# Kernel tuning notes

Hardware: AMD Instinct MI355X
Metric: run time of the kernel (lower is better)

Reference implementation:

```python
import jax, jax.numpy as jnp
import numpy as np

B, N, C = 2, 2048, 768
H, HD = 12, 64
HID = 3072
LN_EPS = 1e-5
POL_EPS = 1e-6


def _layer_norm(x, g, b):
    m = jnp.mean(x, axis=-1, keepdims=True)
    v = jnp.mean(jnp.square(x - m), axis=-1, keepdims=True)
    return (x - m) * jax.lax.rsqrt(v + LN_EPS) * g + b


def _softmax_with_policy(attn, policy):
    # attn: [B,H,N,N], policy: [B,N,1]
    n = attn.shape[-1]
    ap = policy.reshape(policy.shape[0], 1, 1, n)  # [B,1,1,N]
    eye = jnp.eye(n, dtype=ap.dtype)[None, None]   # [1,1,N,N]
    ap = ap + (1.0 - ap) * eye                     # always attend to self
    attn = attn - jnp.max(attn, axis=-1, keepdims=True)
    attn = jnp.exp(attn.astype(jnp.float32)) * ap.astype(jnp.float32)
    attn = (attn + POL_EPS / n) / (jnp.sum(attn, axis=-1, keepdims=True) + POL_EPS)
    return attn


def setup_inputs() -> dict:
    key = jax.random.key(0)
    ks = jax.random.split(key, 12)
    s = lambda fan_in: 1.0 / np.sqrt(fan_in)
    x = jax.random.normal(ks[0], (B, N, C), dtype=jnp.float32)
    policy = (jax.random.uniform(ks[1], (B, N, 1)) > 0.5).astype(jnp.float32)
    return {
        "x": x,
        "policy": policy,
        "ln1_g": jnp.ones((C,), jnp.float32),
        "ln1_b": jnp.zeros((C,), jnp.float32),
        "qkv_w": jax.random.uniform(ks[2], (3 * H * HD, C), jnp.float32, -s(C), s(C)),
        "proj_w": jax.random.uniform(ks[3], (C, H * HD), jnp.float32, -s(H * HD), s(H * HD)),
        "proj_b": jnp.zeros((C,), jnp.float32),
        "ln2_g": jnp.ones((C,), jnp.float32),
        "ln2_b": jnp.zeros((C,), jnp.float32),
        "fc1_w": jax.random.uniform(ks[4], (HID, C), jnp.float32, -s(C), s(C)),
        "fc1_b": jnp.zeros((HID,), jnp.float32),
        "fc2_w": jax.random.uniform(ks[5], (C, HID), jnp.float32, -s(HID), s(HID)),
        "fc2_b": jnp.zeros((C,), jnp.float32),
    }


def reference(x, policy, ln1_g, ln1_b, qkv_w, proj_w, proj_b, ln2_g, ln2_b, fc1_w, fc1_b, fc2_w, fc2_b):
    b, n, c = x.shape
    scale = HD ** -0.5
    # --- attention branch (pre-LN) ---
    h = _layer_norm(x, ln1_g, ln1_b)
    qkv = (h @ qkv_w.T).reshape(b, n, 3, H, HD).transpose(2, 0, 3, 1, 4)  # [3,B,H,N,hd]
    q, k, v = qkv[0], qkv[1], qkv[2]
    attn = jnp.einsum("bhqd,bhkd->bhqk", q * scale, k)
    attn = _softmax_with_policy(attn, policy).astype(x.dtype)
    o = jnp.einsum("bhqk,bhkd->bhqd", attn, v).transpose(0, 2, 1, 3).reshape(b, n, H * HD)
    x = x + (o @ proj_w.T + proj_b)  # skip_lam = 1.0, dropout/drop_path = identity
    # --- MLP branch (pre-LN) ---
    h = _layer_norm(x, ln2_g, ln2_b)
    h = jax.nn.gelu(h @ fc1_w.T + fc1_b, approximate=False)  # torch nn.GELU = exact erf
    x = x + (h @ fc2_w.T + fc2_b)
    return x
```

## Files before the change

### kernel.cpp

```cpp
#include <hip/hip_runtime.h>

typedef unsigned short u16;
typedef unsigned int u32;
typedef float f32x4 __attribute__((ext_vector_type(4)));
typedef float f32x16 __attribute__((ext_vector_type(16)));
typedef __bf16 bf16x8 __attribute__((ext_vector_type(8)));
typedef u16 u16x4v __attribute__((ext_vector_type(4)));
typedef u32 u32x2 __attribute__((ext_vector_type(2)));
typedef u32 u32x4 __attribute__((ext_vector_type(4)));

#define NHEAD 12
#define NN 2048
#define CC 768

#define GLOBAL_AS __attribute__((address_space(1)))
#define LDS_AS __attribute__((address_space(3)))

__device__ __forceinline__ u16 tobf(float f) {
  __bf16 h = (__bf16)f;
  return __builtin_bit_cast(u16, h);
}
__device__ __forceinline__ float bf2f(u16 h) {
  u32 u = ((u32)h) << 16;
  return __builtin_bit_cast(float, u);
}
__device__ __forceinline__ u32 cvtpk(float lo, float hi) {
  u32 r;
  asm("v_cvt_pk_bf16_f32 %0, %1, %2" : "=v"(r) : "v"(lo), "v"(hi));
  return r;
}
__device__ __forceinline__ void plswap(u32& a, u32& b) {
  asm volatile("v_permlane32_swap_b32 %0, %1" : "+v"(a), "+v"(b));
}
__device__ __forceinline__ void plswapf(float& a, float& b) {
  asm volatile("v_permlane32_swap_b32 %0, %1" : "+v"(a), "+v"(b));
}
__device__ __forceinline__ float gelu_erf(float v) {
  float y = fabsf(v) * 0.70710678118654752f;
  float t = __builtin_amdgcn_rcpf(fmaf(0.3275911f, y, 1.f));
  float p = fmaf(1.061405429f, t, -1.453152027f);
  p = fmaf(p, t, 1.421413741f);
  p = fmaf(p, t, -0.284496736f);
  p = fmaf(p, t, 0.254829592f);
  p = p * t;
  float e = __builtin_amdgcn_exp2f(-y * y * 1.44269504f);
  float er = fmaf(-p, e, 1.f);
  er = (v < 0.f) ? -er : er;
  return 0.5f * v * (1.f + er);
}

#define N4_QKV 442368
#define N4_PROJ 147456
#define N4_FC 589824
__global__ __launch_bounds__(256) void cvt4_kernel(
    const float* __restrict__ a, const float* __restrict__ b,
    const float* __restrict__ c, const float* __restrict__ d,
    u16* __restrict__ oa, u16* __restrict__ ob, u16* __restrict__ oc,
    u16* __restrict__ od) {
  int i = blockIdx.x * 256 + threadIdx.x;
  const float* src;
  u16* dst;
  if (i < N4_QKV) {
    src = a; dst = oa;
  } else if (i < N4_QKV + N4_PROJ) {
    i -= N4_QKV; src = b; dst = ob;
  } else if (i < N4_QKV + N4_PROJ + N4_FC) {
    i -= N4_QKV + N4_PROJ; src = c; dst = oc;
  } else {
    i -= N4_QKV + N4_PROJ + N4_FC; src = d; dst = od;
    if (i >= N4_FC) return;
  }
  float4 v = ((const float4*)src)[i];
  u16x4v o = {tobf(v.x), tobf(v.y), tobf(v.z), tobf(v.w)};
  ((u16x4v*)dst)[i] = o;
}

__global__ __launch_bounds__(256) void ln_kernel(const float* __restrict__ x,
                                                 const float* __restrict__ gw,
                                                 const float* __restrict__ bw,
                                                 u16* __restrict__ out) {
  int row = blockIdx.x * 4 + (threadIdx.x >> 6);
  int lane = threadIdx.x & 63;
  const float* xr = x + (size_t)row * CC + lane * 12;
  float v[12];
  *(float4*)&v[0] = *(const float4*)(xr + 0);
  *(float4*)&v[4] = *(const float4*)(xr + 4);
  *(float4*)&v[8] = *(const float4*)(xr + 8);
  float s = 0.f, sq = 0.f;
#pragma unroll
  for (int j = 0; j < 12; ++j) { s += v[j]; sq += v[j] * v[j]; }
#pragma unroll
  for (int o = 1; o < 64; o <<= 1) { s += __shfl_xor(s, o); sq += __shfl_xor(sq, o); }
  float mean = s * (1.f / CC);
  float var = sq * (1.f / CC) - mean * mean;
  float rs = rsqrtf(var + 1e-5f);
  u16 ob[12];
#pragma unroll
  for (int j = 0; j < 12; ++j) {
    int c = lane * 12 + j;
    ob[j] = tobf((v[j] - mean) * rs * gw[c] + bw[c]);
  }
  u32* orow = (u32*)(out + (size_t)row * CC + lane * 12);
#pragma unroll
  for (int j = 0; j < 6; ++j) orow[j] = (u32)ob[2 * j] | ((u32)ob[2 * j + 1] << 16);
}

template <int BM, int BN, int OB, int HASB, int ACT, int RES>
__global__ __launch_bounds__(256) void gemm_kernel(
    const u16* __restrict__ A, const u16* __restrict__ Bw,
    const float* __restrict__ bias, const float* __restrict__ res,
    void* __restrict__ Cout, int M, int N, int K) {
  constexpr int MW = BM / 2;
  constexpr int MF = MW / 16;
  constexpr int NF = BN / 32;
  __shared__ __align__(16) u16 Alds[BM * 64];
  __shared__ __align__(16) u16 Blds[BN * 64];
  const int tid = threadIdx.x;
  const int lane = tid & 63, wave = tid >> 6;
  const int l15 = lane & 15, g = lane >> 4;
  const int nx = gridDim.x;
  const int flat = blockIdx.y * nx + blockIdx.x;
  const int cpx = (nx * gridDim.y) >> 3;
  const int swz = (flat & 7) * cpx + (flat >> 3);
  const int bm = (swz % nx) * BM, bn = (swz / nx) * BN;
  const int wm = (wave >> 1) * MW, wn = (wave & 1) * (BN / 2);
  f32x4 acc[MF][NF] = {};

  for (int kt = 0; kt < K; kt += 64) {
#pragma unroll
    for (int i = 0; i < BM / 32; ++i) {
      int ob_ = i * 4096 + wave * 1024;
      int lb = ob_ + lane * 16;
      int row = lb >> 7;
      int cb = (lb & 127) ^ ((row & 7) << 4);
      const u16* sa = A + (size_t)(bm + row) * K + kt + (cb >> 1);
      __builtin_amdgcn_global_load_lds((const GLOBAL_AS void*)sa,
                                       (LDS_AS void*)(Alds + (ob_ >> 1)), 16, 0, 0);
    }
#pragma unroll
    for (int i = 0; i < BN / 32; ++i) {
      int ob_ = i * 4096 + wave * 1024;
      int lb = ob_ + lane * 16;
      int row = lb >> 7;
      int cb = (lb & 127) ^ ((row & 7) << 4);
      const u16* sb = Bw + (size_t)(bn + row) * K + kt + (cb >> 1);
      __builtin_amdgcn_global_load_lds((const GLOBAL_AS void*)sb,
                                       (LDS_AS void*)(Blds + (ob_ >> 1)), 16, 0, 0);
    }
    __syncthreads();
#pragma unroll
    for (int ks = 0; ks < 2; ++ks) {
      bf16x8 af[MF], bfr[NF];
#pragma unroll
      for (int mi = 0; mi < MF; ++mi) {
        int row = wm + mi * 16 + l15;
        int cb = (ks * 64 + g * 16) ^ ((row & 7) << 4);
        af[mi] = *(const bf16x8*)&Alds[row * 64 + (cb >> 1)];
      }
#pragma unroll
// ... 19 lines not shown
      float bs = HASB ? bias[col] : 0.f;
#pragma unroll
      for (int r = 0; r < 4; ++r) {
        int rowm = bm + wm + mi * 16 + g * 4 + r;
        float v = acc[mi][ni][r] + bs;
        if (ACT) v = gelu_erf(v);
        if (RES) v += res[(size_t)rowm * N + col];
        if (OB)
          ((u16*)Cout)[(size_t)rowm * N + col] = tobf(v);
        else
          ((float*)Cout)[(size_t)rowm * N + col] = v;
      }
    }
  }
}

__global__ __launch_bounds__(256) void vsum_kernel(const u16* __restrict__ qkv,
                                                   float* __restrict__ vs) {
  int bh = blockIdx.x, q4 = blockIdx.y;
  int b = bh / NHEAD, h = bh % NHEAD;
  int d = threadIdx.x & 63, part = threadIdx.x >> 6;
  float s = 0.f;
  for (int n = q4 * 512 + part; n < q4 * 512 + 512; n += 4)
    s += bf2f(qkv[(size_t)(b * NN + n) * 2304 + 2 * CC + h * 64 + d]);
  __shared__ float red[256];
  red[threadIdx.x] = s;
  __syncthreads();
  if (threadIdx.x < 64) {
    float t = red[threadIdx.x] + red[threadIdx.x + 64] + red[threadIdx.x + 128] +
              red[threadIdx.x + 192];
    vs[q4 * (24 * 64) + bh * 64 + threadIdx.x] = t;
  }
}

__global__ __launch_bounds__(256) void scan_kernel(const float* __restrict__ policy,
                                                   int* __restrict__ ncbuf,
                                                   int* __restrict__ idxbuf) {
  int b = blockIdx.x, tid = threadIdx.x;
  float pv[8];
  *(float4*)&pv[0] = *(const float4*)&policy[b * NN + tid * 8];
  *(float4*)&pv[4] = *(const float4*)&policy[b * NN + tid * 8 + 4];
  int cnt = 0;
#pragma unroll
  for (int j = 0; j < 8; ++j) cnt += (pv[j] != 0.f) ? 1 : 0;
  __shared__ int sc[256];
  sc[tid] = cnt;
  __syncthreads();
  for (int off = 1; off < 256; off <<= 1) {
    int v = sc[tid];
    int add = (tid >= off) ? sc[tid - off] : 0;
    __syncthreads();
    sc[tid] = v + add;
    __syncthreads();
  }
  int base = sc[tid] - cnt;
#pragma unroll
  for (int j = 0; j < 8; ++j) {
    if (pv[j] != 0.f) idxbuf[b * NN + base++] = tid * 8 + j;
  }
  if (tid == 255) ncbuf[b] = sc[255];
}

__global__ __launch_bounds__(256) void gather_kernel(const u16* __restrict__ qkv,
                                                     const int* __restrict__ ncbuf,
                                                     const int* __restrict__ idxbuf,
                                                     u16* __restrict__ ckv) {
  int b = blockIdx.y;
  int nc = ncbuf[b];
  int ncp = (nc + 127) & ~127;
  int c = blockIdx.x * 256 + threadIdx.x;
  int j = c / 192, col = (c % 192) * 8;
  if (j >= ncp) return;
  uint4 val = {0, 0, 0, 0};
  if (j < nc) {
    int src = idxbuf[b * NN + j];
    val = *(const uint4*)&qkv[(size_t)(b * NN + src) * 2304 + CC + col];
  }
  *(uint4*)&ckv[(size_t)(b * NN + j) * 1536 + col] = val;
}

#define SCL2E 0.18033688f
#define TRRD(dst, addr, OFF) \
  asm volatile("ds_read_b64_tr_b16 %0, %1 offset:" OFF : "=v"(dst) : "v"(addr))

__global__ __launch_bounds__(128) void attn32_kernel(const u16* __restrict__ qkv,
                                                     const u16* __restrict__ ckv,
                                                     const int* __restrict__ ncbuf,
                                                     const float* __restrict__ policy,
                                                     const float* __restrict__ vsum,
                                                     u16* __restrict__ o) {
  __shared__ __align__(16) u16 Klds[2][4096];
  __shared__ __align__(16) u16 Vlds[2][4096];
  __shared__ float alf[2][32];
  __shared__ float4 alfe[2][32];
  const int bh = blockIdx.y, b = bh / NHEAD, h = bh % NHEAD;
  const int tid = threadIdx.x, lane = tid & 63, w = tid >> 6;
  const int l31 = lane & 31, hp = lane >> 5, b4 = (lane >> 4) & 1;
  const int q0 = blockIdx.x * 64 + w * 32;
  const int nc = ncbuf[b];
  const int ncp = (nc + 127) & ~127;
  const int nt = ncp >> 6;
  const size_t adv = (size_t)64 * 1536;

  bf16x8 qf0, qf1, qf2, qf3;
  {
    const u16* qp = qkv + (size_t)(b * NN + q0 + l31) * 2304 + h * 64 + 8 * hp;
#pragma unroll
    for (int ds = 0; ds < 4; ++ds) {
      bf16x8 r = *(const bf16x8*)(qp + ds * 16);
      bf16x8 oo;
#pragma unroll
      for (int j = 0; j < 8; ++j) oo[j] = (__bf16)((float)r[j] * SCL2E);
      if (ds == 0) qf0 = oo; else if (ds == 1) qf1 = oo; else if (ds == 2) qf2 = oo; else qf3 = oo;
    }
  }

  const u16* ksrc[4];
  const u16* vsrcp[4];
#pragma unroll
  for (int c = 0; c < 4; ++c) {
    int L = c * 128 + w * 64 + lane;
    int lb = L * 16;
    int row = lb >> 7;
    int cb = (lb & 127) ^ ((row & 7) << 4);
    ksrc[c] = ckv + (size_t)(b * NN + row) * 1536 + h * 64 + (cb >> 1);
    int idx0 = L * 8;
    int s0 = idx0 & 15, jj = (idx0 >> 4) & 3, b4v = (idx0 >> 6) & 1,
        pv = (idx0 >> 7) & 1, hv = (idx0 >> 8) & 1, dtv = (idx0 >> 9) & 1,
        mkv = (idx0 >> 10) & 3;
    int key = mkv * 16 + 8 * hv + 4 * pv + jj;
    int d0 = dtv * 32 + 16 * b4v + s0;
    vsrcp[c] = ckv + (size_t)(b * NN + key) * 1536 + CC + h * 64 + d0;
  }
  auto stage = [&](int buf) {
#pragma unroll
    for (int c = 0; c < 4; ++c) {
      __builtin_amdgcn_global_load_lds((const GLOBAL_AS void*)ksrc[c],
                                       (LDS_AS void*)&Klds[buf][c * 1024 + w * 512], 16, 0, 0);
      __builtin_amdgcn_global_load_lds((const GLOBAL_AS void*)vsrcp[c],
                                       (LDS_AS void*)&Vlds[buf][c * 1024 + w * 512], 16, 0, 0);
      ksrc[c] += adv; vsrcp[c] += adv;
    }
  };

  stage(0);
  __syncthreads();

  float m_cur = -3.0e38f, m_true = -3.0e38f, l_run = 0.f;
  f32x16 accd[2] = {};
  const u32 vbase = (u32)(uintptr_t)(LDS_AS u16*)&Vlds[0][0] +
                    (u32)(2 * (lane & 15) + 128 * b4 + 512 * hp);

#pragma unroll 1
  for (int t = 0; t < nt; ++t) {
    const int cur = t & 1;
    if (t < nt - 1) stage(cur ^ 1);

    f32x16 sv0, sv1;
    {
      bf16x8 kf[4];
#pragma unroll
      for (int ds = 0; ds < 4; ++ds) {
        int row = l31;
        int cb = (32 * ds + 16 * hp) ^ ((row & 7) << 4);
        kf[ds] = *(const bf16x8*)((const char*)&Klds[cur][0] + row * 128 + cb);
      }
      f32x16 a = {};
      a = __builtin_amdgcn_mfma_f32_32x32x16_bf16(kf[0], qf0, a, 0, 0, 0);
      a = __builtin_amdgcn_mfma_f32_32x32x16_bf16(kf[1], qf1, a, 0, 0, 0);
      a = __builtin_amdgcn_mfma_f32_32x32x16_bf16(kf[2], qf2, a, 0, 0, 0);
      a = __builtin_amdgcn_mfma_f32_32x32x16_bf16(kf[3], qf3, a, 0, 0, 0);
      sv0 = a;
    }
    {
      bf16x8 kf[4];
#pragma unroll
      for (int ds = 0; ds < 4; ++ds) {
        int row = 32 + l31;
        int cb = (32 * ds + 16 * hp) ^ ((row & 7) << 4);
        kf[ds] = *(const bf16x8*)((const char*)&Klds[cur][0] + row * 128 + cb);
      }
      f32x16 a = {};
      a = __builtin_amdgcn_mfma_f32_32x32x16_bf16(kf[0], qf0, a, 0, 0, 0);
      a = __builtin_amdgcn_mfma_f32_32x32x16_bf16(kf[1], qf1, a, 0, 0, 0);
      a = __builtin_amdgcn_mfma_f32_32x32x16_bf16(kf[2], qf2, a, 0, 0, 0);
      a = __builtin_amdgcn_mfma_f32_32x32x16_bf16(kf[3], qf3, a, 0, 0, 0);
      sv1 = a;
    }

    u32x2 tr[4][2][2];
    {
      u32 vab = vbase + (u32)(cur * 8192);
      TRRD(tr[0][0][0], vab, "0");    TRRD(tr[0][0][1], vab, "256");
      TRRD(tr[0][1][0], vab, "1024"); TRRD(tr[0][1][1], vab, "1280");
      TRRD(tr[1][0][0], vab, "2048"); TRRD(tr[1][0][1], vab, "2304");
      TRRD(tr[1][1][0], vab, "3072"); TRRD(tr[1][1][1], vab, "3328");
      TRRD(tr[2][0][0], vab, "4096"); TRRD(tr[2][0][1], vab, "4352");
      TRRD(tr[3][0][0], vab, "6144"); TRRD(tr[3][0][1], vab, "6400");
      TRRD(tr[2][1][0], vab, "5120"); TRRD(tr[2][1][1], vab, "5376");
      TRRD(tr[3][1][0], vab, "7168"); TRRD(tr[3][1][1], vab, "7424");
    }

    float ta = fmaxf(fmaxf(sv0[0], sv0[1]), sv0[2]);
    float tb = fmaxf(fmaxf(sv0[3], sv0[4]), sv0[5]);
    float tc = fmaxf(fmaxf(sv0[6], sv0[7]), sv0[8]);
    float td = fmaxf(fmaxf(sv0[9], sv0[10]), sv0[11]);
    float te = fmaxf(fmaxf(sv0[12], sv0[13]), sv0[14]);
    float tf = fmaxf(fmaxf(sv0[15], sv1[0]), sv1[1]);
    float tg = fmaxf(fmaxf(sv1[2], sv1[3]), sv1[4]);
    float th = fmaxf(fmaxf(sv1[5], sv1[6]), sv1[7]);
    float ti = fmaxf(fmaxf(sv1[8], sv1[9]), sv1[10]);
    float tj = fmaxf(fmaxf(sv1[11], sv1[12]), sv1[13]);
    float tk = fmaxf(sv1[14], sv1[15]);
    float tmax = fmaxf(fmaxf(fmaxf(fmaxf(ta, tb), fmaxf(tc, td)),
                             fmaxf(fmaxf(te, tf), fmaxf(tg, th))),
                       fmaxf(fmaxf(ti, tj), tk));
    {
      float t1 = tmax, t2 = tmax;
      plswapf(t1, t2);
      tmax = fmaxf(t1, t2);
    }
    m_true = fmaxf(m_true, tmax);
    const bool defer = __all(tmax <= m_cur + 8.f);
    const float m_new = defer ? m_cur : fmaxf(m_cur, tmax);

    const int thr = nc - t * 64;
    float ev[32];
#pragma unroll
    for (int kt = 0; kt < 2; ++kt) {
#pragma unroll
      for (int i = 0; i < 4; ++i) {
#pragma unroll
        for (int rq = 0; rq < 4; ++rq) {
          int r = 4 * i + rq;
          int kidx = kt * 32 + 8 * i + 4 * hp + rq;
          float sval = kt ? sv1[r] : sv0[r];
          float e = __builtin_amdgcn_exp2f(sval - m_new);
          ev[kt * 16 + r] = (kidx < thr) ? e : 0.f;
        }
      }
    }
    u32 wv[16];
#pragma unroll
    for (int j = 0; j < 16; ++j) wv[j] = cvtpk(ev[2 * j], ev[2 * j + 1]);
    float ps[16];
#pragma unroll
    for (int j = 0; j < 16; ++j)
      ps[j] = __builtin_bit_cast(float, wv[j] << 16) +
              __builtin_bit_cast(float, wv[j] & 0xffff0000u);
#pragma unroll
    for (int s = 8; s > 0; s >>= 1)
#pragma unroll
      for (int j = 0; j < s; ++j) ps[j] += ps[j + s];
    float psum = ps[0];
    {
      float s1 = psum, s2 = psum;
      plswapf(s1, s2);
      psum = s1 + s2;
    }
    if (!defer) {
      float alpha = __builtin_amdgcn_exp2f(m_cur - m_new);
      l_run = l_run * alpha + psum;
      m_cur = m_new;
      if (lane < 32) alf[w][lane] = alpha;
      float4 aq0 = *(const float4*)&alf[w][4 * hp];
      float4 aq1 = *(const float4*)&alf[w][8 + 4 * hp];
      float4 aq2 = *(const float4*)&alf[w][16 + 4 * hp];
      float4 aq3 = *(const float4*)&alf[w][24 + 4 * hp];
#pragma unroll
      for (int dt = 0; dt < 2; ++dt) {
#pragma unroll
        for (int rq = 0; rq < 4; ++rq) {
          accd[dt][0 + rq] *= ((const float*)&aq0)[rq];
          accd[dt][4 + rq] *= ((const float*)&aq1)[rq];
          accd[dt][8 + rq] *= ((const float*)&aq2)[rq];
          accd[dt][12 + rq] *= ((const float*)&aq3)[rq];
        }
      }
    } else {
      l_run += psum;
    }

    u32 PK[4][4];
#pragma unroll
    for (int mk = 0; mk < 4; ++mk) {
      int bw_ = 8 * (mk >> 1) + 4 * (mk & 1);
      PK[mk][0] = wv[bw_ + 0];
      PK[mk][1] = wv[bw_ + 1];
      PK[mk][2] = wv[bw_ + 2];
      PK[mk][3] = wv[bw_ + 3];
      plswap(PK[mk][2], PK[mk][0]);
      plswap(PK[mk][3], PK[mk][1]);
    }

    asm volatile("s_waitcnt lgkmcnt(0)" ::: "memory");
    __builtin_amdgcn_sched_barrier(0);

#pragma unroll
    for (int mk = 0; mk < 4; ++mk) {
      u32x4 pk4 = {PK[mk][0], PK[mk][1], PK[mk][2], PK[mk][3]};
      bf16x8 pf = __builtin_bit_cast(bf16x8, pk4);
#pragma unroll
      for (int dt = 0; dt < 2; ++dt) {
        u32x4 vv = {tr[mk][dt][0].x, tr[mk][dt][0].y, tr[mk][dt][1].x, tr[mk][dt][1].y};
        bf16x8 vf = __builtin_bit_cast(bf16x8, vv);
        accd[dt] = __builtin_amdgcn_mfma_f32_32x32x16_bf16(pf, vf, accd[dt], 0, 0, 0);
      }
    }
    __syncthreads();
  }

  float sr = __builtin_amdgcn_exp2f(m_cur - m_true);
  float dp;
  {
    const u16* kp = qkv + (size_t)(b * NN + q0 + l31) * 2304 + CC + h * 64 + 8 * hp;
    float acc_dp = 0.f;
#pragma unroll
    for (int ds = 0; ds < 4; ++ds) {
      bf16x8 kr = *(const bf16x8*)(kp + ds * 16);
      const bf16x8& qv = (ds == 0) ? qf0 : (ds == 1) ? qf1 : (ds == 2) ? qf2 : qf3;
#pragma unroll
      for (int j = 0; j < 8; ++j) acc_dp += (float)qv[j] * (float)kr[j];
    }
    float d2 = acc_dp;
    plswapf(acc_dp, d2);
    dp = acc_dp + d2;
  }
  float pol = policy[b * NN + q0 + l31];
  float ed = (pol == 0.f) ? __builtin_amdgcn_exp2f(dp - m_true) : 0.f;
  if (lane < 32) {
    float4 pk = {l_run * sr, ed, sr, 0.f};
    alfe[w][lane] = pk;
  }
  float vsv0 = vsum[bh * 64 + l31] + vsum[1536 + bh * 64 + l31] +
               vsum[3072 + bh * 64 + l31] + vsum[4608 + bh * 64 + l31];
  float vsv1 = vsum[bh * 64 + 32 + l31] + vsum[1536 + bh * 64 + 32 + l31] +
               vsum[3072 + bh * 64 + 32 + l31] + vsum[4608 + bh * 64 + 32 + l31];
  const float epsn = 1e-6f / (float)NN;
#pragma unroll
  for (int i = 0; i < 4; ++i) {
#pragma unroll
    for (int rq = 0; rq < 4; ++rq) {
      int r = 8 * i + 4 * hp + rq;
      float4 brd = alfe[w][r];
      const u16* vrow = qkv + (size_t)(b * NN + q0 + r) * 2304 + 2 * CC + h * 64;
      float den = brd.x + brd.y + 1e-6f;
      float rden = __builtin_amdgcn_rcpf(den);
#pragma unroll
      for (int dt = 0; dt < 2; ++dt) {
        float vval = bf2f(vrow[dt * 32 + l31]);
        float vsv = dt ? vsv1 : vsv0;
        float num = accd[dt][4 * i + rq] * brd.z + brd.y * vval + epsn * vsv;
        o[(size_t)(b * NN + q0 + r) * CC + h * 64 + dt * 32 + l31] = tobf(num * rden);
      }
    }
  }
}

extern "C" void kernel_launch(void* const* d_in, const int* in_sizes, int n_in,
                              void* d_out, int out_size, void* d_ws, size_t ws_size,
                              hipStream_t stream) {
  const float* x = (const float*)d_in[0];
  const float* policy = (const float*)d_in[1];
  const float* ln1g = (const float*)d_in[2];
  const float* ln1b = (const float*)d_in[3];
  const float* qkvw = (const float*)d_in[4];
  const float* projw = (const float*)d_in[5];
  const float* projb = (const float*)d_in[6];
  const float* ln2g = (const float*)d_in[7];
  const float* ln2b = (const float*)d_in[8];
  const float* fc1w = (const float*)d_in[9];
  const float* fc1b = (const float*)d_in[10];
  const float* fc2w = (const float*)d_in[11];
  const float* fc2b = (const float*)d_in[12];
  float* out = (float*)d_out;

  char* ws = (char*)d_ws;
  size_t off = 0;
  auto alloc = [&](size_t bytes) {
    void* p = ws + off;
    off = (off + bytes + 255) & ~(size_t)255;
    return p;
  };
  u16* wq = (u16*)alloc((size_t)2304 * 768 * 2);
  u16* wp = (u16*)alloc((size_t)768 * 768 * 2);
  u16* w1 = (u16*)alloc((size_t)3072 * 768 * 2);
  u16* w2 = (u16*)alloc((size_t)768 * 3072 * 2);
  u16* hbuf = (u16*)alloc((size_t)4096 * 768 * 2);
  u16* obuf = (u16*)alloc((size_t)4096 * 768 * 2);
  u16* qkv = (u16*)alloc((size_t)4096 * 2304 * 2);
  float* vs = (float*)alloc((size_t)4 * 24 * 64 * 4);
  int* ncbuf = (int*)alloc(2 * sizeof(int));
  int* idxbuf = (int*)alloc((size_t)2 * NN * sizeof(int));
  u16* ckv = (u16*)alloc((size_t)2 * NN * 1536 * 2);
  float* x1 = (float*)alloc((size_t)4096 * 768 * 4);
  u16* f1 = obuf;

  cvt4_kernel<<<6912, 256, 0, stream>>>(qkvw, projw, fc1w, fc2w, wq, wp, w1, w2);

  ln_kernel<<<1024, 256, 0, stream>>>(x, ln1g, ln1b, hbuf);
  gemm_kernel<64, 128, 1, 0, 0, 0><<<dim3(64, 18), 256, 0, stream>>>(
      hbuf, wq, nullptr, nullptr, qkv, 4096, 2304, 768);
  vsum_kernel<<<dim3(24, 4), 256, 0, stream>>>(qkv, vs);
  scan_kernel<<<2, 256, 0, stream>>>(policy, ncbuf, idxbuf);
  gather_kernel<<<dim3(1536, 2), 256, 0, stream>>>(qkv, ncbuf, idxbuf, ckv);
  attn32_kernel<<<dim3(32, 24), 128, 0, stream>>>(qkv, ckv, ncbuf, policy, vs, obuf);
  gemm_kernel<64, 64, 0, 1, 0, 1><<<dim3(64, 12), 256, 0, stream>>>(
      obuf, wp, projb, x, x1, 4096, 768, 768);
  ln_kernel<<<1024, 256, 0, stream>>>(x1, ln2g, ln2b, hbuf);
  gemm_kernel<64, 128, 1, 1, 1, 0><<<dim3(64, 24), 256, 0, stream>>>(
      hbuf, w1, fc1b, nullptr, f1, 4096, 3072, 768);
  gemm_kernel<64, 64, 0, 1, 0, 1><<<dim3(64, 12), 256, 0, stream>>>(
      f1, w2, fc2b, x1, out, 4096, 768, 3072);
}
```

Baseline: 214.5 us.

## Split attention KV range across two blocks and merge partials via atomic counter

```diff
diff --git a/kernel.cpp b/kernel.cpp
--- a/kernel.cpp
+++ b/kernel.cpp
@@ -75,6 +75,11 @@
   ((u16x4v*)dst)[i] = o;
 }
 
+__global__ __launch_bounds__(256) void zero_kernel(int* __restrict__ p, int n) {
+  int i = blockIdx.x * 256 + threadIdx.x;
+  if (i < n) p[i] = 0;
+}
+
 __global__ __launch_bounds__(256) void ln_kernel(const float* __restrict__ x,
                                                  const float* __restrict__ gw,
                                                  const float* __restrict__ bw,
@@ -261,23 +266,26 @@
 #define TRRD(dst, addr, OFF) \
   asm volatile("ds_read_b64_tr_b16 %0, %1 offset:" OFF : "=v"(dst) : "v"(addr))
 
-__global__ __launch_bounds__(128) void attn32_kernel(const u16* __restrict__ qkv,
-                                                     const u16* __restrict__ ckv,
-                                                     const int* __restrict__ ncbuf,
-                                                     const float* __restrict__ policy,
-                                                     const float* __restrict__ vsum,
-                                                     u16* __restrict__ o) {
+__global__ __launch_bounds__(128) void attn32_kernel(
+    const u16* __restrict__ qkv, const u16* __restrict__ ckv,
+    const int* __restrict__ ncbuf, const float* __restrict__ policy,
+    const float* __restrict__ vsum, float* __restrict__ partO,
+    float2* __restrict__ partlm, int* __restrict__ cnt, u16* __restrict__ o) {
   __shared__ __align__(16) u16 Klds[2][4096];
   __shared__ __align__(16) u16 Vlds[2][4096];
   __shared__ float alf[2][32];
   __shared__ float4 alfe[2][32];
+  __shared__ int who;
   const int bh = blockIdx.y, b = bh / NHEAD, h = bh % NHEAD;
+  const int qt = blockIdx.x >> 1, half = blockIdx.x & 1;
   const int tid = threadIdx.x, lane = tid & 63, w = tid >> 6;
   const int l31 = lane & 31, hp = lane >> 5, b4 = (lane >> 4) & 1;
-  const int q0 = blockIdx.x * 64 + w * 32;
+  const int q0 = qt * 64 + w * 32;
   const int nc = ncbuf[b];
   const int ncp = (nc + 127) & ~127;
-  const int nt = ncp >> 6;
+  const int nh = ncp >> 1;
+  const int nt = nh >> 6;
+  const int kv0 = half * nh;
   const size_t adv = (size_t)64 * 1536;
 
   bf16x8 qf0, qf1, qf2, qf3;
@@ -301,14 +309,14 @@
     int lb = L * 16;
     int row = lb >> 7;
     int cb = (lb & 127) ^ ((row & 7) << 4);
-    ksrc[c] = ckv + (size_t)(b * NN + row) * 1536 + h * 64 + (cb >> 1);
+    ksrc[c] = ckv + (size_t)(b * NN + kv0 + row) * 1536 + h * 64 + (cb >> 1);
     int idx0 = L * 8;
     int s0 = idx0 & 15, jj = (idx0 >> 4) & 3, b4v = (idx0 >> 6) & 1,
         pv = (idx0 >> 7) & 1, hv = (idx0 >> 8) & 1, dtv = (idx0 >> 9) & 1,
         mkv = (idx0 >> 10) & 3;
     int key = mkv * 16 + 8 * hv + 4 * pv + jj;
     int d0 = dtv * 32 + 16 * b4v + s0;
-    vsrcp[c] = ckv + (size_t)(b * NN + key) * 1536 + CC + h * 64 + d0;
+    vsrcp[c] = ckv + (size_t)(b * NN + kv0 + key) * 1536 + CC + h * 64 + d0;
   }
   auto stage = [&](int buf) {
 #pragma unroll
@@ -335,6 +343,7 @@
     if (t < nt - 1) stage(cur ^ 1);
 
     f32x16 sv0, sv1;
+    __builtin_amdgcn_s_setprio(1);
     {
       bf16x8 kf[4];
 #pragma unroll
@@ -365,6 +374,7 @@
       a = __builtin_amdgcn_mfma_f32_32x32x16_bf16(kf[3], qf3, a, 0, 0, 0);
       sv1 = a;
     }
+    __builtin_amdgcn_s_setprio(0);
 
     u32x2 tr[4][2][2];
     {
@@ -402,7 +412,7 @@
     const bool defer = __all(tmax <= m_cur + 8.f);
     const float m_new = defer ? m_cur : fmaxf(m_cur, tmax);
 
-    const int thr = nc - t * 64;
+    const int thr = nc - (kv0 + t * 64);
     float ev[32];
 #pragma unroll
     for (int kt = 0; kt < 2; ++kt) {
@@ -474,6 +484,7 @@
     asm volatile("s_waitcnt lgkmcnt(0)" ::: "memory");
     __builtin_amdgcn_sched_barrier(0);
 
+    __builtin_amdgcn_s_setprio(1);
 #pragma unroll
     for (int mk = 0; mk < 4; ++mk) {
       u32x4 pk4 = {PK[mk][0], PK[mk][1], PK[mk][2], PK[mk][3]};
@@ -485,6 +496,7 @@
         accd[dt] = __builtin_amdgcn_mfma_f32_32x32x16_bf16(pf, vf, accd[dt], 0, 0, 0);
       }
     }
+    __builtin_amdgcn_s_setprio(0);
     __syncthreads();
   }
 
@@ -505,11 +517,37 @@
     dp = acc_dp + d2;
   }
   float pol = policy[b * NN + q0 + l31];
-  float ed = (pol == 0.f) ? __builtin_amdgcn_exp2f(dp - m_true) : 0.f;
+  float dpm = (pol == 0.f) ? dp : -3.0e38f;
   if (lane < 32) {
-    float4 pk = {l_run * sr, ed, sr, 0.f};
+    float4 pk = {l_run * sr, dpm, sr, m_true};
     alfe[w][lane] = pk;
   }
+  const int pair = bh * 32 + qt;
+  float* myO = partO + (size_t)(pair * 2 + half) * 4096;
+#pragma unroll
+  for (int i = 0; i < 4; ++i) {
+#pragma unroll
+    for (int rq = 0; rq < 4; ++rq) {
+      int r = 8 * i + 4 * hp + rq;
+      float srr = alfe[w][r].z;
+#pragma unroll
+      for (int dt = 0; dt < 2; ++dt)
+        myO[(w * 32 + r) * 64 + dt * 32 + l31] = accd[dt][4 * i + rq] * srr;
+    }
+  }
+  if (lane < 32) {
+    float2 lm = {l_run * sr, m_true};
+    partlm[(size_t)(pair * 2 + half) * 64 + w * 32 + lane] = lm;
+  }
+  __threadfence();
+  __syncthreads();
+  if (tid == 0) who = atomicAdd(&cnt[pair], 1);
+  __syncthreads();
+  if (who == 0) return;
+  __threadfence();
+
+  const float* oO = partO + (size_t)(pair * 2 + (half ^ 1)) * 4096;
+  const float2* olm = partlm + (size_t)(pair * 2 + (half ^ 1)) * 64;
   float vsv0 = vsum[bh * 64 + l31] + vsum[1536 + bh * 64 + l31] +
                vsum[3072 + bh * 64 + l31] + vsum[4608 + bh * 64 + l31];
   float vsv1 = vsum[bh * 64 + 32 + l31] + vsum[1536 + bh * 64 + 32 + l31] +
@@ -520,15 +558,22 @@
 #pragma unroll
     for (int rq = 0; rq < 4; ++rq) {
       int r = 8 * i + 4 * hp + rq;
+      int rl = w * 32 + r;
       float4 brd = alfe[w][r];
+      float2 lm1 = olm[rl];
+      float ms = fmaxf(brd.w, lm1.y);
+      float w2 = __builtin_amdgcn_exp2f(brd.w - ms);
+      float w1 = __builtin_amdgcn_exp2f(lm1.y - ms);
+      float ed = __builtin_amdgcn_exp2f(brd.y - ms);
       const u16* vrow = qkv + (size_t)(b * NN + q0 + r) * 2304 + 2 * CC + h * 64;
-      float den = brd.x + brd.y + 1e-6f;
+      float den = brd.x * w2 + lm1.x * w1 + ed + 1e-6f;
       float rden = __builtin_amdgcn_rcpf(den);
 #pragma unroll
       for (int dt = 0; dt < 2; ++dt) {
+        float O1 = oO[rl * 64 + dt * 32 + l31];
         float vval = bf2f(vrow[dt * 32 + l31]);
-        float vsv = dt ? vsv1 : vsv0;
-        float num = accd[dt][4 * i + rq] * brd.z + brd.y * vval + epsn * vsv;
+        float num = accd[dt][4 * i + rq] * brd.z * w2 + O1 * w1 + ed * vval +
+                    epsn * (dt ? vsv1 : vsv0);
         o[(size_t)(b * NN + q0 + r) * CC + h * 64 + dt * 32 + l31] = tobf(num * rden);
       }
     }
@@ -571,7 +616,12 @@
   int* ncbuf = (int*)alloc(2 * sizeof(int));
   int* idxbuf = (int*)alloc((size_t)2 * NN * sizeof(int));
   u16* ckv = (u16*)alloc((size_t)2 * NN * 1536 * 2);
-  float* x1 = (float*)alloc((size_t)4096 * 768 * 4);
+  size_t unionOff = off;
+  float* partO = (float*)alloc((size_t)768 * 2 * 4096 * 4);
+  float2* partlm = (float2*)alloc((size_t)768 * 2 * 64 * 8);
+  int* cntb = (int*)alloc(768 * sizeof(int));
+  float* x1 = (float*)(ws + unionOff);
+
   u16* f1 = obuf;
 
   cvt4_kernel<<<6912, 256, 0, stream>>>(qkvw, projw, fc1w, fc2w, wq, wp, w1, w2);
@@ -582,7 +632,9 @@
   vsum_kernel<<<dim3(24, 4), 256, 0, stream>>>(qkv, vs);
   scan_kernel<<<2, 256, 0, stream>>>(policy, ncbuf, idxbuf);
   gather_kernel<<<dim3(1536, 2), 256, 0, stream>>>(qkv, ncbuf, idxbuf, ckv);
-  attn32_kernel<<<dim3(32, 24), 128, 0, stream>>>(qkv, ckv, ncbuf, policy, vs, obuf);
+  zero_kernel<<<3, 256, 0, stream>>>(cntb, 768);
+  attn32_kernel<<<dim3(64, 24), 128, 0, stream>>>(qkv, ckv, ncbuf, policy, vs,
+                                                  partO, partlm, cntb, obuf);
   gemm_kernel<64, 64, 0, 1, 0, 1><<<dim3(64, 12), 256, 0, stream>>>(
       obuf, wp, projb, x, x1, 4096, 768, 768);
   ln_kernel<<<1024, 256, 0, stream>>>(x1, ln2g, ln2b, hbuf);
```

Result: slower. 394.4 us (+83.9%).

## Split attention KV range across two waves per query tile and merge

Applied to the files above, without the earlier changes.

```diff
diff --git a/kernel.cpp b/kernel.cpp
--- a/kernel.cpp
+++ b/kernel.cpp
@@ -260,6 +260,9 @@
 #define SCL2E 0.18033688f
 #define TRRD(dst, addr, OFF) \
   asm volatile("ds_read_b64_tr_b16 %0, %1 offset:" OFF : "=v"(dst) : "v"(addr))
+#define VMW(N)                                          \
+  asm volatile("s_waitcnt vmcnt(" #N ")" ::: "memory"); \
+  __builtin_amdgcn_sched_barrier(0);
 
 __global__ __launch_bounds__(128) void attn32_kernel(const u16* __restrict__ qkv,
                                                      const u16* __restrict__ ckv,
@@ -267,18 +270,21 @@
                                                      const float* __restrict__ policy,
                                                      const float* __restrict__ vsum,
                                                      u16* __restrict__ o) {
-  __shared__ __align__(16) u16 Klds[2][4096];
-  __shared__ __align__(16) u16 Vlds[2][4096];
+  __shared__ __align__(16) u16 Klds[2][2][2048];
+  __shared__ __align__(16) u16 Vlds[2][2][2048];
   __shared__ float alf[2][32];
   __shared__ float4 alfe[2][32];
+  __shared__ float edbuf[32];
   const int bh = blockIdx.y, b = bh / NHEAD, h = bh % NHEAD;
   const int tid = threadIdx.x, lane = tid & 63, w = tid >> 6;
   const int l31 = lane & 31, hp = lane >> 5, b4 = (lane >> 4) & 1;
-  const int q0 = blockIdx.x * 64 + w * 32;
+  const int q0 = blockIdx.x * 32;
   const int nc = ncbuf[b];
   const int ncp = (nc + 127) & ~127;
-  const int nt = ncp >> 6;
-  const size_t adv = (size_t)64 * 1536;
+  const int nh2 = ncp >> 1;
+  const int nt = nh2 >> 5;
+  const int kv0 = w * nh2;
+  const size_t adv = (size_t)32 * 1536;
 
   bf16x8 qf0, qf1, qf2, qf3;
   {
@@ -297,51 +303,55 @@
   const u16* vsrcp[4];
 #pragma unroll
   for (int c = 0; c < 4; ++c) {
-    int L = c * 128 + w * 64 + lane;
+    int L = c * 64 + lane;
     int lb = L * 16;
     int row = lb >> 7;
     int cb = (lb & 127) ^ ((row & 7) << 4);
-    ksrc[c] = ckv + (size_t)(b * NN + row) * 1536 + h * 64 + (cb >> 1);
+    ksrc[c] = ckv + (size_t)(b * NN + kv0 + row) * 1536 + h * 64 + (cb >> 1);
     int idx0 = L * 8;
     int s0 = idx0 & 15, jj = (idx0 >> 4) & 3, b4v = (idx0 >> 6) & 1,
         pv = (idx0 >> 7) & 1, hv = (idx0 >> 8) & 1, dtv = (idx0 >> 9) & 1,
-        mkv = (idx0 >> 10) & 3;
+        mkv = (idx0 >> 10) & 1;
     int key = mkv * 16 + 8 * hv + 4 * pv + jj;
     int d0 = dtv * 32 + 16 * b4v + s0;
-    vsrcp[c] = ckv + (size_t)(b * NN + key) * 1536 + CC + h * 64 + d0;
+    vsrcp[c] = ckv + (size_t)(b * NN + kv0 + key) * 1536 + CC + h * 64 + d0;
   }
   auto stage = [&](int buf) {
 #pragma unroll
     for (int c = 0; c < 4; ++c) {
       __builtin_amdgcn_global_load_lds((const GLOBAL_AS void*)ksrc[c],
-                                       (LDS_AS void*)&Klds[buf][c * 1024 + w * 512], 16, 0, 0);
+                                       (LDS_AS void*)&Klds[w][buf][c * 512], 16, 0, 0);
       __builtin_amdgcn_global_load_lds((const GLOBAL_AS void*)vsrcp[c],
-                                       (LDS_AS void*)&Vlds[buf][c * 1024 + w * 512], 16, 0, 0);
+                                       (LDS_AS void*)&Vlds[w][buf][c * 512], 16, 0, 0);
       ksrc[c] += adv; vsrcp[c] += adv;
     }
   };
 
   stage(0);
-  __syncthreads();
 
   float m_cur = -3.0e38f, m_true = -3.0e38f, l_run = 0.f;
   f32x16 accd[2] = {};
-  const u32 vbase = (u32)(uintptr_t)(LDS_AS u16*)&Vlds[0][0] +
+  const u32 vbase = (u32)(uintptr_t)(LDS_AS u16*)&Vlds[w][0][0] +
                     (u32)(2 * (lane & 15) + 128 * b4 + 512 * hp);
 
+  int cur = 0;
 #pragma unroll 1
   for (int t = 0; t < nt; ++t) {
-    const int cur = t & 1;
-    if (t < nt - 1) stage(cur ^ 1);
-
-    f32x16 sv0, sv1;
+    if (t + 1 < nt) {
+      stage(cur ^ 1);
+      VMW(8);
+    } else {
+      VMW(0);
+    }
+
+    f32x16 sv0;
     {
       bf16x8 kf[4];
 #pragma unroll
       for (int ds = 0; ds < 4; ++ds) {
         int row = l31;
         int cb = (32 * ds + 16 * hp) ^ ((row & 7) << 4);
-        kf[ds] = *(const bf16x8*)((const char*)&Klds[cur][0] + row * 128 + cb);
+        kf[ds] = *(const bf16x8*)((const char*)&Klds[w][cur][0] + row * 128 + cb);
       }
       f32x16 a = {};
       a = __builtin_amdgcn_mfma_f32_32x32x16_bf16(kf[0], qf0, a, 0, 0, 0);
@@ -350,33 +360,14 @@
       a = __builtin_amdgcn_mfma_f32_32x32x16_bf16(kf[3], qf3, a, 0, 0, 0);
       sv0 = a;
     }
+
+    u32x2 tr[2][2][2];
     {
-      bf16x8 kf[4];
-#pragma unroll
-      for (int ds = 0; ds < 4; ++ds) {
-        int row = 32 + l31;
-        int cb = (32 * ds + 16 * hp) ^ ((row & 7) << 4);
-        kf[ds] = *(const bf16x8*)((const char*)&Klds[cur][0] + row * 128 + cb);
-      }
-      f32x16 a = {};
-      a = __builtin_amdgcn_mfma_f32_32x32x16_bf16(kf[0], qf0, a, 0, 0, 0);
-      a = __builtin_amdgcn_mfma_f32_32x32x16_bf16(kf[1], qf1, a, 0, 0, 0);
-      a = __builtin_amdgcn_mfma_f32_32x32x16_bf16(kf[2], qf2, a, 0, 0, 0);
-      a = __builtin_amdgcn_mfma_f32_32x32x16_bf16(kf[3], qf3, a, 0, 0, 0);
-      sv1 = a;
-    }
-
-    u32x2 tr[4][2][2];
-    {
-      u32 vab = vbase + (u32)(cur * 8192);
+      u32 vab = vbase + (u32)(cur * 4096);
       TRRD(tr[0][0][0], vab, "0");    TRRD(tr[0][0][1], vab, "256");
       TRRD(tr[0][1][0], vab, "1024"); TRRD(tr[0][1][1], vab, "1280");
       TRRD(tr[1][0][0], vab, "2048"); TRRD(tr[1][0][1], vab, "2304");
       TRRD(tr[1][1][0], vab, "3072"); TRRD(tr[1][1][1], vab, "3328");
-      TRRD(tr[2][0][0], vab, "4096"); TRRD(tr[2][0][1], vab, "4352");
-      TRRD(tr[3][0][0], vab, "6144"); TRRD(tr[3][0][1], vab, "6400");
-      TRRD(tr[2][1][0], vab, "5120"); TRRD(tr[2][1][1], vab, "5376");
-      TRRD(tr[3][1][0], vab, "7168"); TRRD(tr[3][1][1], vab, "7424");
     }
 
     float ta = fmaxf(fmaxf(sv0[0], sv0[1]), sv0[2]);
@@ -384,15 +375,7 @@
     float tc = fmaxf(fmaxf(sv0[6], sv0[7]), sv0[8]);
     float td = fmaxf(fmaxf(sv0[9], sv0[10]), sv0[11]);
     float te = fmaxf(fmaxf(sv0[12], sv0[13]), sv0[14]);
-    float tf = fmaxf(fmaxf(sv0[15], sv1[0]), sv1[1]);
-    float tg = fmaxf(fmaxf(sv1[2], sv1[3]), sv1[4]);
-    float th = fmaxf(fmaxf(sv1[5], sv1[6]), sv1[7]);
-    float ti = fmaxf(fmaxf(sv1[8], sv1[9]), sv1[10]);
-    float tj = fmaxf(fmaxf(sv1[11], sv1[12]), sv1[13]);
-    float tk = fmaxf(sv1[14], sv1[15]);
-    float tmax = fmaxf(fmaxf(fmaxf(fmaxf(ta, tb), fmaxf(tc, td)),
-                             fmaxf(fmaxf(te, tf), fmaxf(tg, th))),
-                       fmaxf(fmaxf(ti, tj), tk));
+    float tmax = fmaxf(fmaxf(fmaxf(ta, tb), fmaxf(tc, td)), fmaxf(te, sv0[15]));
     {
       float t1 = tmax, t2 = tmax;
       plswapf(t1, t2);
@@ -402,32 +385,28 @@
     const bool defer = __all(tmax <= m_cur + 8.f);
     const float m_new = defer ? m_cur : fmaxf(m_cur, tmax);
 
-    const int thr = nc - t * 64;
-    float ev[32];
-#pragma unroll
-    for (int kt = 0; kt < 2; ++kt) {
-#pragma unroll
-      for (int i = 0; i < 4; ++i) {
-#pragma unroll
-        for (int rq = 0; rq < 4; ++rq) {
-          int r = 4 * i + rq;
-          int kidx = kt * 32 + 8 * i + 4 * hp + rq;
-          float sval = kt ? sv1[r] : sv0[r];
-          float e = __builtin_amdgcn_exp2f(sval - m_new);
-          ev[kt * 16 + r] = (kidx < thr) ? e : 0.f;
-        }
-      }
-    }
-    u32 wv[16];
-#pragma unroll
-    for (int j = 0; j < 16; ++j) wv[j] = cvtpk(ev[2 * j], ev[2 * j + 1]);
-    float ps[16];
-#pragma unroll
-    for (int j = 0; j < 16; ++j)
+    const int thr = nc - (kv0 + t * 32);
+    float ev[16];
+#pragma unroll
+    for (int i = 0; i < 4; ++i) {
+#pragma unroll
+      for (int rq = 0; rq < 4; ++rq) {
+        int r = 4 * i + rq;
+        int kidx = 8 * i + 4 * hp + rq;
+        float e = __builtin_amdgcn_exp2f(sv0[r] - m_new);
+        ev[r] = (kidx < thr) ? e : 0.f;
+      }
+    }
+    u32 wv[8];
+#pragma unroll
+    for (int j = 0; j < 8; ++j) wv[j] = cvtpk(ev[2 * j], ev[2 * j + 1]);
+    float ps[8];
+#pragma unroll
+    for (int j = 0; j < 8; ++j)
       ps[j] = __builtin_bit_cast(float, wv[j] << 16) +
               __builtin_bit_cast(float, wv[j] & 0xffff0000u);
 #pragma unroll
-    for (int s = 8; s > 0; s >>= 1)
+    for (int s = 4; s > 0; s >>= 1)
 #pragma unroll
       for (int j = 0; j < s; ++j) ps[j] += ps[j + s];
     float psum = ps[0];
@@ -459,23 +438,19 @@
       l_run += psum;
     }
 
-    u32 PK[4][4];
-#pragma unroll
-    for (int mk = 0; mk < 4; ++mk) {
-      int bw_ = 8 * (mk >> 1) + 4 * (mk & 1);
-      PK[mk][0] = wv[bw_ + 0];
-      PK[mk][1] = wv[bw_ + 1];
-      PK[mk][2] = wv[bw_ + 2];
-      PK[mk][3] = wv[bw_ + 3];
-      plswap(PK[mk][2], PK[mk][0]);
-      plswap(PK[mk][3], PK[mk][1]);
-    }
+    u32 PK[2][4];
+    PK[0][0] = wv[0]; PK[0][1] = wv[1]; PK[0][2] = wv[2]; PK[0][3] = wv[3];
+    PK[1][0] = wv[4]; PK[1][1] = wv[5]; PK[1][2] = wv[6]; PK[1][3] = wv[7];
+    plswap(PK[0][2], PK[0][0]);
+    plswap(PK[0][3], PK[0][1]);
+    plswap(PK[1][2], PK[1][0]);
+    plswap(PK[1][3], PK[1][1]);
 
     asm volatile("s_waitcnt lgkmcnt(0)" ::: "memory");
     __builtin_amdgcn_sched_barrier(0);
 
 #pragma unroll
-    for (int mk = 0; mk < 4; ++mk) {
+    for (int mk = 0; mk < 2; ++mk) {
       u32x4 pk4 = {PK[mk][0], PK[mk][1], PK[mk][2], PK[mk][3]};
       bf16x8 pf = __builtin_bit_cast(bf16x8, pk4);
 #pragma unroll
@@ -485,7 +460,7 @@
         accd[dt] = __builtin_amdgcn_mfma_f32_32x32x16_bf16(pf, vf, accd[dt], 0, 0, 0);
       }
     }
-    __syncthreads();
+    cur ^= 1;
   }
 
   float sr = __builtin_amdgcn_exp2f(m_cur - m_true);
@@ -505,33 +480,43 @@
     dp = acc_dp + d2;
   }
   float pol = policy[b * NN + q0 + l31];
-  float ed = (pol == 0.f) ? __builtin_amdgcn_exp2f(dp - m_true) : 0.f;
+  if (w == 0 && lane < 32) edbuf[l31] = (pol == 0.f) ? dp : -3.0e38f;
   if (lane < 32) {
-    float4 pk = {l_run * sr, ed, sr, 0.f};
+    float4 pk = {l_run * sr, 0.f, sr, m_true};
     alfe[w][lane] = pk;
   }
-  float vsv0 = vsum[bh * 64 + l31] + vsum[1536 + bh * 64 + l31] +
-               vsum[3072 + bh * 64 + l31] + vsum[4608 + bh * 64 + l31];
-  float vsv1 = vsum[bh * 64 + 32 + l31] + vsum[1536 + bh * 64 + 32 + l31] +
-               vsum[3072 + bh * 64 + 32 + l31] + vsum[4608 + bh * 64 + 32 + l31];
-  const float epsn = 1e-6f / (float)NN;
+  float* Op = (float*)&Klds[w][0][0];
 #pragma unroll
   for (int i = 0; i < 4; ++i) {
 #pragma unroll
     for (int rq = 0; rq < 4; ++rq) {
       int r = 8 * i + 4 * hp + rq;
-      float4 brd = alfe[w][r];
-      const u16* vrow = qkv + (size_t)(b * NN + q0 + r) * 2304 + 2 * CC + h * 64;
-      float den = brd.x + brd.y + 1e-6f;
-      float rden = __builtin_amdgcn_rcpf(den);
-#pragma unroll
-      for (int dt = 0; dt < 2; ++dt) {
-        float vval = bf2f(vrow[dt * 32 + l31]);
-        float vsv = dt ? vsv1 : vsv0;
-        float num = accd[dt][4 * i + rq] * brd.z + brd.y * vval + epsn * vsv;
-        o[(size_t)(b * NN + q0 + r) * CC + h * 64 + dt * 32 + l31] = tobf(num * rden);
-      }
-    }
+      float srr = alfe[w][r].z;
+#pragma unroll
+      for (int dt = 0; dt < 2; ++dt)
+        Op[r * 64 + dt * 32 + l31] = accd[dt][4 * i + rq] * srr;
+    }
+  }
+  __syncthreads();
+
+  const float* Op0 = (const float*)&Klds[0][0][0];
+  const float* Op1 = (const float*)&Klds[1][0][0];
+  const int d = tid & 63, rh = tid >> 6;
+  float vsv = vsum[bh * 64 + d] + vsum[1536 + bh * 64 + d] +
+              vsum[3072 + bh * 64 + d] + vsum[4608 + bh * 64 + d];
+  const float epsn = 1e-6f / (float)NN;
+#pragma unroll 1
+  for (int r = rh * 16; r < rh * 16 + 16; ++r) {
+    float4 a0 = alfe[0][r];
+    float4 a1 = alfe[1][r];
+    float ms = fmaxf(a0.w, a1.w);
+    float w0 = __builtin_amdgcn_exp2f(a0.w - ms);
+    float w1e = __builtin_amdgcn_exp2f(a1.w - ms);
+    float edv = __builtin_amdgcn_exp2f(edbuf[r] - ms);
+    float den = a0.x * w0 + a1.x * w1e + edv + 1e-6f;
+    float vval = bf2f(qkv[(size_t)(b * NN + q0 + r) * 2304 + 2 * CC + h * 64 + d]);
+    float num = Op0[r * 64 + d] * w0 + Op1[r * 64 + d] * w1e + edv * vval + epsn * vsv;
+    o[(size_t)(b * NN + q0 + r) * CC + h * 64 + d] = tobf(num * __builtin_amdgcn_rcpf(den));
   }
 }
 
@@ -582,7 +567,7 @@
   vsum_kernel<<<dim3(24, 4), 256, 0, stream>>>(qkv, vs);
   scan_kernel<<<2, 256, 0, stream>>>(policy, ncbuf, idxbuf);
   gather_kernel<<<dim3(1536, 2), 256, 0, stream>>>(qkv, ncbuf, idxbuf, ckv);
-  attn32_kernel<<<dim3(32, 24), 128, 0, stream>>>(qkv, ckv, ncbuf, policy, vs, obuf);
+  attn32_kernel<<<dim3(64, 24), 128, 0, stream>>>(qkv, ckv, ncbuf, policy, vs, obuf);
   gemm_kernel<64, 64, 0, 1, 0, 1><<<dim3(64, 12), 256, 0, stream>>>(
       obuf, wp, projb, x, x1, 4096, 768, 768);
   ln_kernel<<<1024, 256, 0, stream>>>(x1, ln2g, ln2b, hbuf);
```

After: 232.6 us. 1.08x slower.

## Split attention KV range across two wave pairs with LDS merge of partial softmax

Applied to the files above, without the earlier changes.

```diff
diff --git a/kernel.cpp b/kernel.cpp
--- a/kernel.cpp
+++ b/kernel.cpp
@@ -261,28 +261,32 @@
 #define TRRD(dst, addr, OFF) \
   asm volatile("ds_read_b64_tr_b16 %0, %1 offset:" OFF : "=v"(dst) : "v"(addr))
 
-__global__ __launch_bounds__(128) void attn32_kernel(const u16* __restrict__ qkv,
+__global__ __launch_bounds__(256) void attn32_kernel(const u16* __restrict__ qkv,
                                                      const u16* __restrict__ ckv,
                                                      const int* __restrict__ ncbuf,
                                                      const float* __restrict__ policy,
                                                      const float* __restrict__ vsum,
                                                      u16* __restrict__ o) {
-  __shared__ __align__(16) u16 Klds[2][4096];
-  __shared__ __align__(16) u16 Vlds[2][4096];
-  __shared__ float alf[2][32];
-  __shared__ float4 alfe[2][32];
+  __shared__ __align__(16) u16 smem[2][2][2][2048];
+  __shared__ float alf[4][32];
+  __shared__ float4 alfe[4][32];
+  __shared__ float edbuf[64];
   const int bh = blockIdx.y, b = bh / NHEAD, h = bh % NHEAD;
   const int tid = threadIdx.x, lane = tid & 63, w = tid >> 6;
+  const int tm = w >> 1, tw = w & 1;
   const int l31 = lane & 31, hp = lane >> 5, b4 = (lane >> 4) & 1;
-  const int q0 = blockIdx.x * 64 + w * 32;
+  const int q0 = blockIdx.x * 64;
+  const int qrow = q0 + tw * 32 + l31;
   const int nc = ncbuf[b];
   const int ncp = (nc + 127) & ~127;
-  const int nt = ncp >> 6;
+  const int nh = ncp >> 1;
+  const int nt = nh >> 6;
+  const int kv0 = tm * nh;
   const size_t adv = (size_t)64 * 1536;
 
   bf16x8 qf0, qf1, qf2, qf3;
   {
-    const u16* qp = qkv + (size_t)(b * NN + q0 + l31) * 2304 + h * 64 + 8 * hp;
+    const u16* qp = qkv + (size_t)(b * NN + qrow) * 2304 + h * 64 + 8 * hp;
 #pragma unroll
     for (int ds = 0; ds < 4; ++ds) {
       bf16x8 r = *(const bf16x8*)(qp + ds * 16);
@@ -297,26 +301,27 @@
   const u16* vsrcp[4];
 #pragma unroll
   for (int c = 0; c < 4; ++c) {
-    int L = c * 128 + w * 64 + lane;
+    int L = c * 128 + tw * 64 + lane;
     int lb = L * 16;
     int row = lb >> 7;
     int cb = (lb & 127) ^ ((row & 7) << 4);
-    ksrc[c] = ckv + (size_t)(b * NN + row) * 1536 + h * 64 + (cb >> 1);
+    ksrc[c] = ckv + (size_t)(b * NN + kv0 + row) * 1536 + h * 64 + (cb >> 1);
     int idx0 = L * 8;
     int s0 = idx0 & 15, jj = (idx0 >> 4) & 3, b4v = (idx0 >> 6) & 1,
         pv = (idx0 >> 7) & 1, hv = (idx0 >> 8) & 1, dtv = (idx0 >> 9) & 1,
         mkv = (idx0 >> 10) & 3;
     int key = mkv * 16 + 8 * hv + 4 * pv + jj;
     int d0 = dtv * 32 + 16 * b4v + s0;
-    vsrcp[c] = ckv + (size_t)(b * NN + key) * 1536 + CC + h * 64 + d0;
+    vsrcp[c] = ckv + (size_t)(b * NN + kv0 + key) * 1536 + CC + h * 64 + d0;
   }
   auto stage = [&](int buf) {
 #pragma unroll
     for (int c = 0; c < 4; ++c) {
+      int e0 = c * 1024 + tw * 512 + lane * 8;
       __builtin_amdgcn_global_load_lds((const GLOBAL_AS void*)ksrc[c],
-                                       (LDS_AS void*)&Klds[buf][c * 1024 + w * 512], 16, 0, 0);
+                                       (LDS_AS void*)&smem[tm][0][buf][e0], 16, 0, 0);
       __builtin_amdgcn_global_load_lds((const GLOBAL_AS void*)vsrcp[c],
-                                       (LDS_AS void*)&Vlds[buf][c * 1024 + w * 512], 16, 0, 0);
+                                       (LDS_AS void*)&smem[tm][1][buf][e0], 16, 0, 0);
       ksrc[c] += adv; vsrcp[c] += adv;
     }
   };
@@ -326,14 +331,15 @@
 
   float m_cur = -3.0e38f, m_true = -3.0e38f, l_run = 0.f;
   f32x16 accd[2] = {};
-  const u32 vbase = (u32)(uintptr_t)(LDS_AS u16*)&Vlds[0][0] +
-                    (u32)(2 * (lane & 15) + 128 * b4 + 512 * hp);
-
+  const u32 vbase0 = (u32)(uintptr_t)(LDS_AS u16*)&smem[tm][1][0][0] +
+                     (u32)(2 * (lane & 15) + 128 * b4 + 512 * hp);
+
+  int cur = 0;
 #pragma unroll 1
   for (int t = 0; t < nt; ++t) {
-    const int cur = t & 1;
     if (t < nt - 1) stage(cur ^ 1);
 
+    const char* Kb = (const char*)&smem[tm][0][cur][0];
     f32x16 sv0, sv1;
     {
       bf16x8 kf[4];
@@ -341,7 +347,7 @@
       for (int ds = 0; ds < 4; ++ds) {
         int row = l31;
         int cb = (32 * ds + 16 * hp) ^ ((row & 7) << 4);
-        kf[ds] = *(const bf16x8*)((const char*)&Klds[cur][0] + row * 128 + cb);
+        kf[ds] = *(const bf16x8*)(Kb + row * 128 + cb);
       }
       f32x16 a = {};
       a = __builtin_amdgcn_mfma_f32_32x32x16_bf16(kf[0], qf0, a, 0, 0, 0);
@@ -356,7 +362,7 @@
       for (int ds = 0; ds < 4; ++ds) {
         int row = 32 + l31;
         int cb = (32 * ds + 16 * hp) ^ ((row & 7) << 4);
-        kf[ds] = *(const bf16x8*)((const char*)&Klds[cur][0] + row * 128 + cb);
+        kf[ds] = *(const bf16x8*)(Kb + row * 128 + cb);
       }
       f32x16 a = {};
       a = __builtin_amdgcn_mfma_f32_32x32x16_bf16(kf[0], qf0, a, 0, 0, 0);
@@ -368,14 +374,15 @@
 
     u32x2 tr[4][2][2];
     {
-      u32 vab = vbase + (u32)(cur * 8192);
+      u32 vab = vbase0 + (u32)(cur * 8192);
+      vab = vbase0 + (u32)(cur * 4096);
       TRRD(tr[0][0][0], vab, "0");    TRRD(tr[0][0][1], vab, "256");
       TRRD(tr[0][1][0], vab, "1024"); TRRD(tr[0][1][1], vab, "1280");
       TRRD(tr[1][0][0], vab, "2048"); TRRD(tr[1][0][1], vab, "2304");
       TRRD(tr[1][1][0], vab, "3072"); TRRD(tr[1][1][1], vab, "3328");
       TRRD(tr[2][0][0], vab, "4096"); TRRD(tr[2][0][1], vab, "4352");
+      TRRD(tr[2][1][0], vab, "5120"); TRRD(tr[2][1][1], vab, "5376");
       TRRD(tr[3][0][0], vab, "6144"); TRRD(tr[3][0][1], vab, "6400");
-      TRRD(tr[2][1][0], vab, "5120"); TRRD(tr[2][1][1], vab, "5376");
       TRRD(tr[3][1][0], vab, "7168"); TRRD(tr[3][1][1], vab, "7424");
     }
 
@@ -402,7 +409,7 @@
     const bool defer = __all(tmax <= m_cur + 8.f);
     const float m_new = defer ? m_cur : fmaxf(m_cur, tmax);
 
-    const int thr = nc - t * 64;
+    const int thr = nc - (kv0 + t * 64);
     float ev[32];
 #pragma unroll
     for (int kt = 0; kt < 2; ++kt) {
@@ -486,12 +493,13 @@
       }
     }
     __syncthreads();
+    cur ^= 1;
   }
 
   float sr = __builtin_amdgcn_exp2f(m_cur - m_true);
   float dp;
   {
-    const u16* kp = qkv + (size_t)(b * NN + q0 + l31) * 2304 + CC + h * 64 + 8 * hp;
+    const u16* kp = qkv + (size_t)(b * NN + qrow) * 2304 + CC + h * 64 + 8 * hp;
     float acc_dp = 0.f;
 #pragma unroll
     for (int ds = 0; ds < 4; ++ds) {
@@ -504,34 +512,46 @@
     plswapf(acc_dp, d2);
     dp = acc_dp + d2;
   }
-  float pol = policy[b * NN + q0 + l31];
-  float ed = (pol == 0.f) ? __builtin_amdgcn_exp2f(dp - m_true) : 0.f;
+  float pol = policy[b * NN + qrow];
+  if (tm == 0 && lane < 32) edbuf[tw * 32 + l31] = (pol == 0.f) ? dp : -3.0e38f;
   if (lane < 32) {
-    float4 pk = {l_run * sr, ed, sr, 0.f};
+    float4 pk = {l_run * sr, 0.f, sr, m_true};
     alfe[w][lane] = pk;
   }
-  float vsv0 = vsum[bh * 64 + l31] + vsum[1536 + bh * 64 + l31] +
-               vsum[3072 + bh * 64 + l31] + vsum[4608 + bh * 64 + l31];
-  float vsv1 = vsum[bh * 64 + 32 + l31] + vsum[1536 + bh * 64 + 32 + l31] +
-               vsum[3072 + bh * 64 + 32 + l31] + vsum[4608 + bh * 64 + 32 + l31];
+  __syncthreads();
+  float* Op = (float*)&smem[tm][0][0][0];
+#pragma unroll
+  for (int i = 0; i < 4; ++i) {
+#pragma unroll
+    for (int rq = 0; rq < 4; ++rq) {
+      int rloc = 8 * i + 4 * hp + rq;
+      float srr = alfe[w][rloc].z;
+      int r = tw * 32 + rloc;
+#pragma unroll
+      for (int dt = 0; dt < 2; ++dt)
+        Op[r * 64 + dt * 32 + l31] = accd[dt][4 * i + rq] * srr;
+    }
+  }
+  __syncthreads();
+
+  const float* Op0 = (const float*)&smem[0][0][0][0];
+  const float* Op1 = (const float*)&smem[1][0][0][0];
+  const int d = tid & 63, rh = tid >> 6;
+  float vsv = vsum[bh * 64 + d] + vsum[1536 + bh * 64 + d] +
+              vsum[3072 + bh * 64 + d] + vsum[4608 + bh * 64 + d];
   const float epsn = 1e-6f / (float)NN;
-#pragma unroll
-  for (int i = 0; i < 4; ++i) {
-#pragma unroll
-    for (int rq = 0; rq < 4; ++rq) {
-      int r = 8 * i + 4 * hp + rq;
-      float4 brd = alfe[w][r];
-      const u16* vrow = qkv + (size_t)(b * NN + q0 + r) * 2304 + 2 * CC + h * 64;
-      float den = brd.x + brd.y + 1e-6f;
-      float rden = __builtin_amdgcn_rcpf(den);
-#pragma unroll
-      for (int dt = 0; dt < 2; ++dt) {
-        float vval = bf2f(vrow[dt * 32 + l31]);
-        float vsv = dt ? vsv1 : vsv0;
-        float num = accd[dt][4 * i + rq] * brd.z + brd.y * vval + epsn * vsv;
-        o[(size_t)(b * NN + q0 + r) * CC + h * 64 + dt * 32 + l31] = tobf(num * rden);
-      }
-    }
+#pragma unroll 1
+  for (int r = rh * 16; r < rh * 16 + 16; ++r) {
+    float4 a0 = alfe[(r >> 5)][r & 31];
+    float4 a1 = alfe[2 + (r >> 5)][r & 31];
+    float ms = fmaxf(a0.w, a1.w);
+    float w0 = __builtin_amdgcn_exp2f(a0.w - ms);
+    float w1e = __builtin_amdgcn_exp2f(a1.w - ms);
+    float edv = __builtin_amdgcn_exp2f(edbuf[r] - ms);
+    float den = a0.x * w0 + a1.x * w1e + edv + 1e-6f;
+    float vval = bf2f(qkv[(size_t)(b * NN + q0 + r) * 2304 + 2 * CC + h * 64 + d]);
+    float num = Op0[r * 64 + d] * w0 + Op1[r * 64 + d] * w1e + edv * vval + epsn * vsv;
+    o[(size_t)(b * NN + q0 + r) * CC + h * 64 + d] = tobf(num * __builtin_amdgcn_rcpf(den));
   }
 }
 
@@ -582,7 +602,7 @@
   vsum_kernel<<<dim3(24, 4), 256, 0, stream>>>(qkv, vs);
   scan_kernel<<<2, 256, 0, stream>>>(policy, ncbuf, idxbuf);
   gather_kernel<<<dim3(1536, 2), 256, 0, stream>>>(qkv, ncbuf, idxbuf, ckv);
-  attn32_kernel<<<dim3(32, 24), 128, 0, stream>>>(qkv, ckv, ncbuf, policy, vs, obuf);
+  attn32_kernel<<<dim3(32, 24), 256, 0, stream>>>(qkv, ckv, ncbuf, policy, vs, obuf);
   gemm_kernel<64, 64, 0, 1, 0, 1><<<dim3(64, 12), 256, 0, stream>>>(
       obuf, wp, projb, x, x1, 4096, 768, 768);
   ln_kernel<<<1024, 256, 0, stream>>>(x1, ln2g, ln2b, hbuf);
```

New measurement: 224.0 us. +4.5%, slower.
